# Kernel tuning notes

Hardware: AMD Instinct MI355X
Metric: run time of the kernel (lower is better)

## Reference

```python
import jax, jax.numpy as jnp
import numpy as np

B, N, U, K = 2, 768, 64, 8
IN = 2 * U + K  # 136
SLOPE = 0.01    # torch LeakyReLU default


def setup_inputs() -> dict:
    key = jax.random.key(0)
    ks = jax.random.split(key, 12)
    seq_embed = jax.random.normal(ks[0], (B, N, U), dtype=jnp.float32)
    vals = jax.random.uniform(ks[1], (N, N, K), dtype=jnp.float32)
    edge = (jax.random.uniform(ks[2], (N, N)) < 0.05) | jnp.eye(N, dtype=bool)
    relational_encoding = vals * edge[:, :, None].astype(jnp.float32)
    s = 0.05
    inp = {"seq_embed": seq_embed, "relational_encoding": relational_encoding}
    # per-hop MLP params: hop k has Linear(IN,IN) then Linear(IN,1); W stored (in,out)
    inp["w1_1"] = jax.random.normal(ks[3], (IN, IN), dtype=jnp.float32) * s
    inp["b1_1"] = jax.random.normal(ks[4], (IN,), dtype=jnp.float32) * s
    inp["w1_2"] = jax.random.normal(ks[5], (IN, 1), dtype=jnp.float32) * s
    inp["b1_2"] = jax.random.normal(ks[6], (1,), dtype=jnp.float32) * s
    inp["w2_1"] = jax.random.normal(ks[7], (IN, IN), dtype=jnp.float32) * s
    inp["b2_1"] = jax.random.normal(ks[8], (IN,), dtype=jnp.float32) * s
    inp["w2_2"] = jax.random.normal(ks[9], (IN, 1), dtype=jnp.float32) * s
    inp["b2_2"] = jax.random.normal(ks[10], (1,), dtype=jnp.float32) * s
    return inp


def _fwd(seq_embed, relational_encoding, hop_params):
    mask = (relational_encoding.sum(-1) > 0).astype(seq_embed.dtype)  # (N,N)
    D = mask.sum(-1)  # (N,) row degree
    rel = relational_encoding[None]  # (1,N,N,K) broadcast over batch
    x = seq_embed
    for layers in hop_params:
        b, n, u = x.shape
        e_i = jnp.broadcast_to(x[:, :, None, :], (b, n, n, u))  # row embed
        e_j = jnp.broadcast_to(x[:, None, :, :], (b, n, n, u))  # col embed
        seq_combined = jnp.concatenate([e_i, e_j], axis=-1)     # (B,N,N,2U)
        combined = jnp.concatenate(
            [seq_combined, jnp.broadcast_to(rel, (b, n, n, rel.shape[-1]))], axis=-1)
        combined = combined * mask[None, :, :, None]
        w = combined
        for (W, bb) in layers:
            w = jax.nn.leaky_relu(w @ W + bb, SLOPE)
        w = w[..., 0] * mask[None]                 # (B,N,N)
        scaled = w / D[None, :, None]              # divide each row i by D[i]
        # weighted neighbor embeds = scaled * e_j, summed over dim 1 (rows)
        x = jnp.einsum('bij,biju->bju', scaled, e_j)
    return x


def reference(seq_embed, relational_encoding, w1_1, b1_1, w1_2, b1_2,
              w2_1, b2_1, w2_2, b2_2):
    hop_params = [[(w1_1, b1_1), (w1_2, b1_2)], [(w2_1, b2_1), (w2_2, b2_2)]]
    return _fwd(seq_embed, relational_encoding, hop_params)
```

## Files before the change

kernel.cpp:

```cpp
#include <hip/hip_runtime.h>

#define NN 768
#define UU 64
#define KK 8
#define INF 136
#define BB 2
#define SLOPE 0.01f
#define CAP 80
#define NSLOT (NN*CAP)
#define NP 4
#define PSTRIDE 1552

__device__ __forceinline__ float lrelu(float x) { return x > 0.f ? x : SLOPE * x; }


__device__ __forceinline__ void pre_rows(int r4, const float* __restrict__ x,
                                         const float* __restrict__ W,
                                         float* __restrict__ A, float* __restrict__ Bv,
                                         float (*xs)[UU], int tid) {
    { int rr = tid >> 6, u = tid & 63;
      xs[rr][u] = x[(size_t)(r4 + rr) * UU + u]; }
    __syncthreads();
    int m = tid;
    if (m < INF) {
        float a[4] = {0.f,0.f,0.f,0.f}, bv[4] = {0.f,0.f,0.f,0.f};
        for (int u = 0; u < UU; u++) {
            float wa = W[u * INF + m];
            float wb = W[(UU + u) * INF + m];
#pragma unroll
            for (int r = 0; r < 4; r++) { a[r] += xs[r][u] * wa; bv[r] += xs[r][u] * wb; }
        }
#pragma unroll
        for (int r = 0; r < 4; r++) {
            A [(size_t)(r4 + r) * INF + m] = a[r];
            Bv[(size_t)(r4 + r) * INF + m] = bv[r];
        }
    }
}

__global__ void __launch_bounds__(256) k_setup(
        const float* __restrict__ rel, const float* __restrict__ seq,
        const float* __restrict__ W1, const float* __restrict__ W2,
        int* __restrict__ recs, int* __restrict__ rowcnt,
        float* __restrict__ A, float* __restrict__ Bv,
        float* __restrict__ P2, float* __restrict__ Q2,
        float* __restrict__ s1p, float4* __restrict__ outz,
        float* __restrict__ relc) {
    __shared__ float xs[4][UU];
    __shared__ int wcnt[4];
    int blk = blockIdx.x;
    int tid = threadIdx.x;

    if (blk >= NN) {
        int g = blk - NN;
        bool h2 = g >= 384;
        if (h2) g -= 384;
        int zi = g * 256 + tid;
        if (h2) {
            if (zi < BB * NN * UU / 4) outz[zi] = make_float4(0.f, 0.f, 0.f, 0.f);
        } else {
            if (zi < NP * PSTRIDE) s1p[zi] = 0.f;
        }
        pre_rows(g * 4, seq, h2 ? W2 : W1, h2 ? P2 : A, h2 ? Q2 : Bv, xs, tid);
        return;
    }

    int i = blk;
    int w = tid >> 6, lane = tid & 63;
    int j0 = w * 192;
    float4 ra4[3], rb4[3];
    float sums[3];
#pragma unroll
    for (int it = 0; it < 3; it++) {
        int j = j0 + it * 64 + lane;
        const float4* rp = (const float4*)(rel + (size_t)(i * NN + j) * KK);
        ra4[it] = rp[0]; rb4[it] = rp[1];
        sums[it] = ra4[it].x + ra4[it].y + ra4[it].z + ra4[it].w
                 + rb4[it].x + rb4[it].y + rb4[it].z + rb4[it].w;
    }
    int cnt = 0;
    int pos[3];
    bool act[3];
#pragma unroll
    for (int it = 0; it < 3; it++) {
        act[it] = sums[it] > 0.f;
        unsigned long long m = __ballot(act[it]);
        pos[it] = cnt + __popcll(m & ((1ull << lane) - 1));
        cnt += __popcll(m);
    }
    if (lane == 0) wcnt[w] = cnt;
    __syncthreads();
    int prefix = 0, total = 0;
#pragma unroll
    for (int ww = 0; ww < 4; ww++) {
        int c = wcnt[ww];
        total += c;
        if (ww < w) prefix += c;
    }
    if (tid == 0) rowcnt[i] = total < CAP ? total : CAP;
#pragma unroll
    for (int it = 0; it < 3; it++) {
        if (act[it]) {
            int rp = prefix + pos[it];
            if (rp < CAP) {
                recs[i * CAP + rp] = j0 + it * 64 + lane;
                float4* rc = (float4*)(relc + ((size_t)i * CAP + rp) * 8);
                rc[0] = ra4[it]; rc[1] = rb4[it];
            }
        }
    }
}

template<bool H2>
__global__ void __launch_bounds__(256) k_hop(
        const int* __restrict__ recs, const int* __restrict__ rowcnt,
        const float* __restrict__ relc,
        const float* __restrict__ Ar, const float* __restrict__ Br,
        const float* __restrict__ W1, const float* __restrict__ b1,
        const float* __restrict__ w2, const float* __restrict__ b2,
        const float* __restrict__ sc, float* __restrict__ sp,
        const float* __restrict__ seq, float* __restrict__ out) {
    int lane = threadIdx.x & 63;
    int wid = (blockIdx.x * blockDim.x + threadIdx.x) >> 6;
    const int WPR = CAP / 8;
    int i = wid / WPR;
    int w0 = (wid - i * WPR) * 8;
    int cnt = rowcnt[i];
    if (w0 >= cnt) return;
    int nt = cnt - w0; if (nt > 8) nt = 8;

    int hl = lane & 31, b = lane >> 5;
    int e0 = hl, e1 = 32 + hl, e2 = 64 + hl, e3 = 96 + hl, e4 = 128 + (hl & 7);

    const float* W1R = W1 + 128 * INF;
    float wr0[8], wr1[8], wr2[8], wr3[8], wr4[8];
#pragma unroll
    for (int k = 0; k < 8; k++) {
        const float* Wk = W1R + k * INF;
        wr0[k] = Wk[e0]; wr1[k] = Wk[e1]; wr2[k] = Wk[e2]; wr3[k] = Wk[e3]; wr4[k] = Wk[e4];
    }
    float bb0 = b1[e0], bb1 = b1[e1], bb2 = b1[e2], bb3 = b1[e3], bb4 = b1[e4];
    float w20 = w2[e0], w21 = w2[e1], w22 = w2[e2], w23 = w2[e3];
    float w24 = (hl < 8) ? w2[e4] : 0.f;
    float b2v = b2[0];
    float di = 1.0f / (float)cnt;

    const float* Ai = Ar + ((size_t)b * NN + i) * INF;
    float ai0 = Ai[e0], ai1 = Ai[e1], ai2 = Ai[e2], ai3 = Ai[e3], ai4 = Ai[e4];
    if (H2) {
        float si = 0.f;
#pragma unroll
        for (int p = 0; p < NP; p++) si += sc[p * PSTRIDE + b * NN + i];
        ai0 *= si; ai1 *= si; ai2 *= si; ai3 *= si; ai4 *= si;
    }

    float* s = sp + (wid & (NP - 1)) * PSTRIDE + b * NN;

    int4 q0 = *(const int4*)(recs + i * CAP + w0);
    int4 q1 = *(const int4*)(recs + i * CAP + w0 + 4);
    int jj[8] = {q0.x, q0.y, q0.z, q0.w, q1.x, q1.y, q1.z, q1.w};
    const float4* rc = (const float4*)(relc + ((size_t)i * CAP + w0) * 8);

#pragma unroll
    for (int t = 0; t < 8; t++) {
        if (t >= nt) break;
        int j = jj[t];
        float4 ra = rc[2 * t];
        float4 rb = rc[2 * t + 1];
        float rv[8] = {ra.x, ra.y, ra.z, ra.w, rb.x, rb.y, rb.z, rb.w};
        float r0 = bb0, r1 = bb1, r2 = bb2, r3 = bb3, r4 = bb4;
#pragma unroll
        for (int k = 0; k < 8; k++) {
            r0 += rv[k] * wr0[k]; r1 += rv[k] * wr1[k]; r2 += rv[k] * wr2[k];
            r3 += rv[k] * wr3[k]; r4 += rv[k] * wr4[k];
        }
        const float* Bj = Br + ((size_t)b * NN + j) * INF;
        float sj = 1.f;
        if (H2) {
            sj = 0.f;
#pragma unroll
            for (int p = 0; p < NP; p++) sj += sc[p * PSTRIDE + b * NN + j];
        }
        float dot = lrelu(r0 + ai0 + sj * Bj[e0]) * w20
                  + lrelu(r1 + ai1 + sj * Bj[e1]) * w21
                  + lrelu(r2 + ai2 + sj * Bj[e2]) * w22
                  + lrelu(r3 + ai3 + sj * Bj[e3]) * w23
                  + lrelu(r4 + ai4 + sj * Bj[e4]) * w24;
#pragma unroll
        for (int off = 16; off; off >>= 1) dot += __shfl_xor(dot, off, 64);
        float c = lrelu(dot + b2v) * di;
        if (H2) {
            float val = c * sj;
            const float* sq = seq + ((size_t)b * NN + j) * UU;
            float* op = out + ((size_t)b * NN + j) * UU;
            atomicAdd(&op[hl],      val * sq[hl]);
            atomicAdd(&op[32 + hl], val * sq[32 + hl]);
        } else {
            if (hl == 0) atomicAdd(&s[j], c);
        }
    }
}

extern "C" void kernel_launch(void* const* d_in, const int* in_sizes, int n_in,
                              void* d_out, int out_size, void* d_ws, size_t ws_size,
                              hipStream_t stream) {
    const float* seq  = (const float*)d_in[0];
    const float* rel  = (const float*)d_in[1];
    const float* w1_1 = (const float*)d_in[2];
    const float* b1_1 = (const float*)d_in[3];
    const float* w1_2 = (const float*)d_in[4];
    const float* b1_2 = (const float*)d_in[5];
    const float* w2_1 = (const float*)d_in[6];
    const float* b2_1 = (const float*)d_in[7];
    const float* w2_2 = (const float*)d_in[8];
    const float* b2_2 = (const float*)d_in[9];
    float* out = (float*)d_out;

    char* ws = (char*)d_ws;
    float* s1p   = (float*)(ws + 0);
    int* rowcnt  = (int*)  (ws + 49664);
    float* A     = (float*)(ws + 52736);
    float* Bv    = (float*)(ws + 888320);
    float* P2    = (float*)(ws + 1723904);
    float* Q2    = (float*)(ws + 2559488);
    int* recs    = (int*)  (ws + 3395072);
    float* relc  = (float*)(ws + 3640832);

    k_setup<<<NN + 768, 256, 0, stream>>>(rel, seq, w1_1, w2_1, recs, rowcnt,
                                          A, Bv, P2, Q2, s1p, (float4*)out, relc);
    k_hop<false><<<NSLOT / 32, 256, 0, stream>>>(recs, rowcnt, relc, A, Bv,
                                                 w1_1, b1_1, w1_2, b1_2,
                                                 nullptr, s1p, nullptr, nullptr);
    k_hop<true><<<NSLOT / 32, 256, 0, stream>>>(recs, rowcnt, relc, P2, Q2,
                                                w2_1, b2_1, w2_2, b2_2,
                                                s1p, s1p, seq, out);
}
```

Before: 134.9 us.

## Build column-major edge lists in hop 1 and gather hop 2 per column

Hop 1 now also scatters each edge into a per-column edge list with relation values, using an atomic counter per column. Hop 2 becomes a gather kernel, one block per output node j, that sums the scaled weights over incoming edges and writes out[j] directly. This removes the zeroing of the output and the per-element float atomics on the output from hop 2. The cost is extra scattered writes and atomics in hop 1. The per-row inverse degree is also precomputed in setup from the uncapped count.

```diff
diff --git a/kernel.cpp b/kernel.cpp
--- a/kernel.cpp
+++ b/kernel.cpp
@@ -41,10 +41,10 @@
 __global__ void __launch_bounds__(256) k_setup(
         const float* __restrict__ rel, const float* __restrict__ seq,
         const float* __restrict__ W1, const float* __restrict__ W2,
-        int* __restrict__ recs, int* __restrict__ rowcnt,
+        int* __restrict__ recs, int* __restrict__ rowcnt, float* __restrict__ dinv,
         float* __restrict__ A, float* __restrict__ Bv,
         float* __restrict__ P2, float* __restrict__ Q2,
-        float* __restrict__ s1p, float4* __restrict__ outz,
+        float* __restrict__ s1p, int* __restrict__ colcnt,
         float* __restrict__ relc) {
     __shared__ float xs[4][UU];
     __shared__ int wcnt[4];
@@ -56,11 +56,8 @@
         bool h2 = g >= 384;
         if (h2) g -= 384;
         int zi = g * 256 + tid;
-        if (h2) {
-            if (zi < BB * NN * UU / 4) outz[zi] = make_float4(0.f, 0.f, 0.f, 0.f);
-        } else {
-            if (zi < NP * PSTRIDE) s1p[zi] = 0.f;
-        }
+        if (h2) { if (zi < NN) colcnt[zi] = 0; }
+        else    { if (zi < NP * PSTRIDE) s1p[zi] = 0.f; }
         pre_rows(g * 4, seq, h2 ? W2 : W1, h2 ? P2 : A, h2 ? Q2 : Bv, xs, tid);
         return;
     }
@@ -97,7 +94,10 @@
         total += c;
         if (ww < w) prefix += c;
     }
-    if (tid == 0) rowcnt[i] = total < CAP ? total : CAP;
+    if (tid == 0) {
+        rowcnt[i] = total < CAP ? total : CAP;
+        dinv[i] = 1.0f / (float)total;
+    }
 #pragma unroll
     for (int it = 0; it < 3; it++) {
         if (act[it]) {
@@ -111,15 +111,14 @@
     }
 }
 
-template<bool H2>
-__global__ void __launch_bounds__(256) k_hop(
+__global__ void __launch_bounds__(256) k_hop1(
         const int* __restrict__ recs, const int* __restrict__ rowcnt,
-        const float* __restrict__ relc,
+        const float* __restrict__ dinv, const float* __restrict__ relc,
         const float* __restrict__ Ar, const float* __restrict__ Br,
         const float* __restrict__ W1, const float* __restrict__ b1,
         const float* __restrict__ w2, const float* __restrict__ b2,
-        const float* __restrict__ sc, float* __restrict__ sp,
-        const float* __restrict__ seq, float* __restrict__ out) {
+        float* __restrict__ sp, int* __restrict__ colcnt,
+        int* __restrict__ recs_col, float* __restrict__ relc_col) {
     int lane = threadIdx.x & 63;
     int wid = (blockIdx.x * blockDim.x + threadIdx.x) >> 6;
     const int WPR = CAP / 8;
@@ -143,16 +142,10 @@
     float w20 = w2[e0], w21 = w2[e1], w22 = w2[e2], w23 = w2[e3];
     float w24 = (hl < 8) ? w2[e4] : 0.f;
     float b2v = b2[0];
-    float di = 1.0f / (float)cnt;
+    float di = dinv[i];
 
     const float* Ai = Ar + ((size_t)b * NN + i) * INF;
     float ai0 = Ai[e0], ai1 = Ai[e1], ai2 = Ai[e2], ai3 = Ai[e3], ai4 = Ai[e4];
-    if (H2) {
-        float si = 0.f;
-#pragma unroll
-        for (int p = 0; p < NP; p++) si += sc[p * PSTRIDE + b * NN + i];
-        ai0 *= si; ai1 *= si; ai2 *= si; ai3 *= si; ai4 *= si;
-    }
 
     float* s = sp + (wid & (NP - 1)) * PSTRIDE + b * NN;
 
@@ -167,6 +160,14 @@
         int j = jj[t];
         float4 ra = rc[2 * t];
         float4 rb = rc[2 * t + 1];
+        if (lane == 0) {
+            int cp = atomicAdd(&colcnt[j], 1);
+            if (cp < CAP) {
+                recs_col[j * CAP + cp] = i;
+                float4* dst = (float4*)(relc_col + ((size_t)j * CAP + cp) * 8);
+                dst[0] = ra; dst[1] = rb;
+            }
+        }
         float rv[8] = {ra.x, ra.y, ra.z, ra.w, rb.x, rb.y, rb.z, rb.w};
         float r0 = bb0, r1 = bb1, r2 = bb2, r3 = bb3, r4 = bb4;
 #pragma unroll
@@ -175,29 +176,81 @@
             r3 += rv[k] * wr3[k]; r4 += rv[k] * wr4[k];
         }
         const float* Bj = Br + ((size_t)b * NN + j) * INF;
-        float sj = 1.f;
-        if (H2) {
-            sj = 0.f;
-#pragma unroll
-            for (int p = 0; p < NP; p++) sj += sc[p * PSTRIDE + b * NN + j];
-        }
-        float dot = lrelu(r0 + ai0 + sj * Bj[e0]) * w20
-                  + lrelu(r1 + ai1 + sj * Bj[e1]) * w21
-                  + lrelu(r2 + ai2 + sj * Bj[e2]) * w22
-                  + lrelu(r3 + ai3 + sj * Bj[e3]) * w23
-                  + lrelu(r4 + ai4 + sj * Bj[e4]) * w24;
+        float dot = lrelu(r0 + ai0 + Bj[e0]) * w20
+                  + lrelu(r1 + ai1 + Bj[e1]) * w21
+                  + lrelu(r2 + ai2 + Bj[e2]) * w22
+                  + lrelu(r3 + ai3 + Bj[e3]) * w23
+                  + lrelu(r4 + ai4 + Bj[e4]) * w24;
 #pragma unroll
         for (int off = 16; off; off >>= 1) dot += __shfl_xor(dot, off, 64);
-        float c = lrelu(dot + b2v) * di;
-        if (H2) {
-            float val = c * sj;
-            const float* sq = seq + ((size_t)b * NN + j) * UU;
-            float* op = out + ((size_t)b * NN + j) * UU;
-            atomicAdd(&op[hl],      val * sq[hl]);
-            atomicAdd(&op[32 + hl], val * sq[32 + hl]);
-        } else {
-            if (hl == 0) atomicAdd(&s[j], c);
-        }
+        if (hl == 0) atomicAdd(&s[j], lrelu(dot + b2v) * di);
+    }
+}
+
+__global__ void __launch_bounds__(256) k_hop2c(
+        const int* __restrict__ recs_col, const int* __restrict__ colcnt,
+        const float* __restrict__ relc_col, const float* __restrict__ dinv,
+        const float* __restrict__ s1p,
+        const float* __restrict__ P2, const float* __restrict__ Q2,
+        const float* __restrict__ W, const float* __restrict__ b1,
+        const float* __restrict__ w2, const float* __restrict__ b2,
+        const float* __restrict__ seq, float* __restrict__ out) {
+    __shared__ float part[4];
+    int j = blockIdx.x;
+    int tid = threadIdx.x;
+    int w = tid >> 6, lane = tid & 63;
+    int b = w >> 1, half = w & 1;
+    int e0 = lane, e1 = 64 + lane, e2 = 128 + (lane & 7);
+
+    const float* WR = W + 128 * INF;
+    float wr0[8], wr1[8], wr2[8];
+#pragma unroll
+    for (int k = 0; k < 8; k++) {
+        const float* Wk = WR + k * INF;
+        wr0[k] = Wk[e0]; wr1[k] = Wk[e1]; wr2[k] = Wk[e2];
+    }
+    float bb0 = b1[e0], bb1 = b1[e1], bb2 = b1[e2];
+    float w20 = w2[e0], w21 = w2[e1], w22 = (lane < 8) ? w2[e2] : 0.f;
+    float b2v = b2[0];
+
+    float sjj = 0.f;
+#pragma unroll
+    for (int p = 0; p < NP; p++) sjj += s1p[p * PSTRIDE + b * NN + j];
+    const float* Qj = Q2 + ((size_t)b * NN + j) * INF;
+    float bc0 = Qj[e0] * sjj, bc1 = Qj[e1] * sjj, bc2 = Qj[e2] * sjj;
+
+    int cnt = colcnt[j]; if (cnt > CAP) cnt = CAP;
+    float acc = 0.f;
+#pragma unroll 2
+    for (int r = half; r < cnt; r += 2) {
+        int i = recs_col[j * CAP + r];
+        const float4* rp = (const float4*)(relc_col + ((size_t)j * CAP + r) * 8);
+        float4 ra = rp[0], rb = rp[1];
+        float rv[8] = {ra.x, ra.y, ra.z, ra.w, rb.x, rb.y, rb.z, rb.w};
+        float r0 = bb0, r1 = bb1, r2 = bb2;
+#pragma unroll
+        for (int k = 0; k < 8; k++) {
+            r0 += rv[k] * wr0[k]; r1 += rv[k] * wr1[k]; r2 += rv[k] * wr2[k];
+        }
+        float si = 0.f;
+#pragma unroll
+        for (int p = 0; p < NP; p++) si += s1p[p * PSTRIDE + b * NN + i];
+        const float* Pi = P2 + ((size_t)b * NN + i) * INF;
+        float a0 = Pi[e0] * si, a1 = Pi[e1] * si, a2 = Pi[e2] * si;
+        float dot = lrelu(r0 + a0 + bc0) * w20
+                  + lrelu(r1 + a1 + bc1) * w21
+                  + lrelu(r2 + a2 + bc2) * w22;
+#pragma unroll
+        for (int off = 32; off; off >>= 1) dot += __shfl_xor(dot, off, 64);
+        acc += dinv[i] * lrelu(dot + b2v);
+    }
+    if (lane == 0) part[w] = acc;
+    __syncthreads();
+    if (half == 0) {
+        float s2 = part[2 * b] + part[2 * b + 1];
+        float f = sjj * s2;
+        size_t base = ((size_t)b * NN + j) * UU;
+        out[base + lane] = seq[base + lane] * f;
     }
 }
 
@@ -217,21 +270,24 @@
     float* out = (float*)d_out;
 
     char* ws = (char*)d_ws;
-    float* s1p   = (float*)(ws + 0);
-    int* rowcnt  = (int*)  (ws + 49664);
-    float* A     = (float*)(ws + 52736);
-    float* Bv    = (float*)(ws + 888320);
-    float* P2    = (float*)(ws + 1723904);
-    float* Q2    = (float*)(ws + 2559488);
-    int* recs    = (int*)  (ws + 3395072);
-    float* relc  = (float*)(ws + 3640832);
-
-    k_setup<<<NN + 768, 256, 0, stream>>>(rel, seq, w1_1, w2_1, recs, rowcnt,
-                                          A, Bv, P2, Q2, s1p, (float4*)out, relc);
-    k_hop<false><<<NSLOT / 32, 256, 0, stream>>>(recs, rowcnt, relc, A, Bv,
-                                                 w1_1, b1_1, w1_2, b1_2,
-                                                 nullptr, s1p, nullptr, nullptr);
-    k_hop<true><<<NSLOT / 32, 256, 0, stream>>>(recs, rowcnt, relc, P2, Q2,
-                                                w2_1, b2_1, w2_2, b2_2,
-                                                s1p, s1p, seq, out);
-}
+    float* s1p     = (float*)(ws + 0);
+    int*   colcnt  = (int*)  (ws + 24832);
+    int*   rowcnt  = (int*)  (ws + 27904);
+    float* dinv    = (float*)(ws + 30976);
+    float* A       = (float*)(ws + 34048);
+    float* Bv      = (float*)(ws + 869632);
+    float* P2      = (float*)(ws + 1705216);
+    float* Q2      = (float*)(ws + 2540800);
+    int*   recs    = (int*)  (ws + 3376384);
+    float* relc    = (float*)(ws + 3622144);
+    int*   recs_col= (int*)  (ws + 5588224);
+    float* relc_col= (float*)(ws + 5833984);
+
+    k_setup<<<NN + 768, 256, 0, stream>>>(rel, seq, w1_1, w2_1, recs, rowcnt, dinv,
+                                          A, Bv, P2, Q2, s1p, colcnt, relc);
+    k_hop1<<<NSLOT / 32, 256, 0, stream>>>(recs, rowcnt, dinv, relc, A, Bv,
+                                           w1_1, b1_1, w1_2, b1_2,
+                                           s1p, colcnt, recs_col, relc_col);
+    k_hop2c<<<NN, 256, 0, stream>>>(recs_col, colcnt, relc_col, dinv, s1p,
+                                    P2, Q2, w2_1, b2_1, w2_2, b2_2, seq, out);
+}
```

Result: slower. 140.4 us (+4.1%).
